# Performance work log

Measured on AMD Instinct MI355X. Metric: run time of the kernel, lower is better.

The kernel has to match this reference:

```python
import jax, jax.numpy as jnp
import numpy as np

NB_ATOMS = 128
NB_CH = 1
ATOM = 12          # atom_size
BATCH = 8
HW = 75            # -> 64x64 patch grid
LAM = 0.1          # soft-threshold level of the L1 proximal
UNROLL = 2         # unroll_steps
FISTA_ITERS = 15   # fixed inner FISTA iterations (replaces res-based stop)


def _prox(u):
    # soft-thresholding (prox of lam*||.||_1)
    return jnp.sign(u) * jnp.maximum(jnp.abs(u) - LAM, 0.0)


def _conv(x, w):
    # valid cross-correlation, NCHW / OIHW (== F.conv2d)
    return jax.lax.conv_general_dilated(x, w, (1, 1), 'VALID',
                                        dimension_numbers=('NCHW', 'OIHW', 'NCHW'))


def _fold(patches, H, W):
    # patches: [B, Ph, Pw, a, a] -> overlap-add to [B, 1, H, W] (== F.fold)
    B, Ph, Pw, a, _ = patches.shape
    out = jnp.zeros((B, H, W), patches.dtype)
    for di in range(a):              # fixed small kernel loop (a*a = 144 slots)
        for dj in range(a):
            out = out.at[:, di:di + Ph, dj:dj + Pw].add(patches[:, :, :, di, dj])
    return out[:, None]


def _fista(c0, X, q, mu):
    # standard FISTA on 0.5*||D^T c - y_patch||^2 + lam*||c||_1 with step mu
    def body(i, st):
        c, z, t = st
        cn = _prox(z - (z @ X - q) * mu)
        tn = (1.0 + jnp.sqrt(1.0 + 4.0 * t * t)) / 2.0
        zn = cn + ((t - 1.0) / tn) * (cn - c)
        return (cn, zn, tn)
    c, _, _ = jax.lax.fori_loop(0, FISTA_ITERS, body, (c0, c0, jnp.float32(1.0)))
    return c


def setup_inputs() -> dict:
    key = jax.random.key(0)
    k1, k2 = jax.random.split(key)
    y = jax.random.normal(k1, (BATCH, NB_CH, HW, HW), dtype=jnp.float32)
    atoms = jax.random.normal(k2, (NB_ATOMS, NB_CH, ATOM, ATOM), dtype=jnp.float32) / 1500.0
    beta = jnp.float32(0.1)
    mu = jnp.float32(1.0)
    return {"y": y, "atoms": atoms, "beta": beta, "mu": mu}


def reference(y, atoms, beta, mu):
    B, C, H, W = y.shape
    N, a = atoms.shape[0], atoms.shape[-1]
    beta = jax.nn.relu(beta)
    mu = jax.nn.relu(mu)
    # normalize atoms: zero-mean, unit L2 rows, then spectral norm / sqrt(mu)
    A = atoms - atoms.mean(axis=(1, 2, 3), keepdims=True)
    Af = A.reshape(N, -1)
    Af = Af / jnp.linalg.norm(Af, axis=1, keepdims=True)
    Af = Af / (jnp.linalg.norm(Af, ord=2) * jnp.sqrt(mu))
    atoms_n = Af.reshape(N, C, a, a)
    X = Af @ Af.T                                   # [N, N] gram
    Ph, Pw = H - a + 1, W - a + 1
    n_patch = B * Ph * Pw
    mean_filter = jnp.ones((1, 1, a, a), y.dtype) / (a * a)
    patch_mean = _conv(y, mean_filter).reshape(n_patch, 1, 1, 1)
    divisors = _fold(jnp.ones((B, Ph, Pw, a, a), y.dtype), H, W)  # overlap counts
    goal = y
    c = jnp.zeros((n_patch, N), y.dtype)
    sg = jax.lax.stop_gradient
    for _ in range(UNROLL):
        q = _conv(goal, atoms_n).transpose(0, 2, 3, 1).reshape(n_patch, N)
        cf = sg(_fista(sg(c), sg(X), sg(q), sg(mu)))   # torch.no_grad inner solve
        cf = _prox(cf - (cf @ X - q) * mu)             # one differentiable step
        pred = jnp.einsum('pn,ncij->pcij', cf, atoms_n) + patch_mean  # [P,1,a,a]
        pred = _fold(pred.reshape(B, Ph, Pw, a, a), H, W)
        goal = (y + beta * pred) / (1.0 + beta * divisors)
        c = cf
    return goal
```

## Files before the change

kernel.cpp:

```cpp
#include <hip/hip_runtime.h>
#include <stdint.h>

#define AA 144
#define LAM 0.1f

#define OFS_SC    0
#define OFS_AF1   64
#define OFS_G     36928
#define OFS_S0    53312
#define OFS_S1    69696
#define OFS_X     86080
#define OFS_PM    139328
#define OFS_GOAL  172096
#define OFS_CF    4411456
#define OFS_PRED  8605760
#define OFS_ATB   OFS_S0
#define OFS_ANTB  OFS_S1


typedef __attribute__((ext_vector_type(8))) short short8_t;
typedef __attribute__((ext_vector_type(4))) float f32x4;
typedef __attribute__((ext_vector_type(2))) float f32x2;
typedef __attribute__((ext_vector_type(4))) uint32_t u32x4;

__device__ __forceinline__ unsigned short f2bf(float f) {
    union { float f; uint32_t u; } x; x.f = f;
    uint32_t u = x.u;
    return (unsigned short)((u + 0x7FFFu + ((u >> 16) & 1u)) >> 16);
}
__device__ __forceinline__ unsigned short f2bh(float f) {
    union { float f; uint32_t u; } x; x.f = f;
    return (unsigned short)((x.u + 0x8000u) >> 16);
}
__device__ __forceinline__ float bf2f(unsigned short u) {
    union { float f; uint32_t i; } x; x.i = ((uint32_t)u) << 16; return x.f;
}
__device__ __forceinline__ uint32_t pack_bf(float a, float b) {
    union { float f; uint32_t u; } xa, xb; xa.f = a; xb.f = b;
    return __builtin_amdgcn_perm(xb.u + 0x8000u, xa.u + 0x8000u, 0x07060302u);
}
__device__ __forceinline__ uint32_t cvt_pk(float a, float b) {
    uint32_t r;
    asm("v_cvt_pk_bf16_f32 %0, %1, %2" : "=v"(r) : "v"(a), "v"(b));
    return r;
}

#define PSTR 136
__global__ __launch_bounds__(1024) void k_setup(const float* atoms, const float* mu_p,
                                                float* ws, const float* y) {
    __shared__ unsigned short ABf[128 * 168];
    __shared__ unsigned short Pb[2][128 * PSTR];
    __shared__ float tr_arr[10];
    __shared__ float v[128];
    __shared__ float red[256];
    int t = threadIdx.x;
    if (blockIdx.x != 0) {
        int e = (blockIdx.x - 1) * 1024 + t;
        if (e < 45000) ws[OFS_GOAL + e] = y[e];
        if (e < 32768) {
            int b = e >> 12, pi = (e >> 6) & 63, pj = e & 63;
            const float* yb = y + b * 5625;
            float s = 0.f;
            for (int di = 0; di < 12; ++di) {
                const float* row = yb + (pi + di) * 75 + pj;
                #pragma unroll
                for (int dj = 0; dj < 12; ++dj) s += row[dj];
            }
            ws[OFS_PM + e] = s * (1.0f / 144.0f);
        }
        return;
    }
    int lane = t & 63, w = t >> 6;
    int col = lane & 15, quad = lane >> 4;
    if (t < 10) tr_arr[t] = (t == 0) ? 128.0f : 0.f;

    {
        int a = t >> 3, sub = t & 7;
        const float* ap = atoms + a * AA + sub * 18;
        float s = 0.f;
        #pragma unroll
        for (int k = 0; k < 18; ++k) s += ap[k];
        s += __shfl_xor(s, 1, 8); s += __shfl_xor(s, 2, 8); s += __shfl_xor(s, 4, 8);
        float mean = s * (1.0f / 144.0f);
        float ss = 0.f;
        #pragma unroll
        for (int k = 0; k < 18; ++k) { float d = ap[k] - mean; ss = fmaf(d, d, ss); }
        ss += __shfl_xor(ss, 1, 8); ss += __shfl_xor(ss, 2, 8); ss += __shfl_xor(ss, 4, 8);
        float rn = 1.0f / sqrtf(ss);
        #pragma unroll
        for (int k = 0; k < 18; ++k) {
            float av = (ap[k] - mean) * rn;
            ws[OFS_AF1 + a * AA + sub * 18 + k] = av;
            ABf[a * 168 + sub * 18 + k] = f2bf(av);
        }
        if (sub == 0) {
            #pragma unroll
            for (int k = AA; k < 160; ++k) ABf[a * 168 + k] = 0;
        }
    }
    __syncthreads();

    {
        uint32_t* D32 = (uint32_t*)Pb[0];
        float* G = ws + OFS_G;
        int mt = w & 7, gh = w >> 3;
        short8_t af[5];
        #pragma unroll
        for (int s = 0; s < 5; ++s)
            af[s] = *(const short8_t*)&ABf[(mt * 16 + col) * 168 + s * 32 + quad * 8];
        #pragma unroll
        for (int gi = 0; gi < 2; ++gi) {
            int g = gh * 2 + gi;
            short8_t b0[5], b1[5];
            #pragma unroll
            for (int s = 0; s < 5; ++s) {
                b0[s] = *(const short8_t*)&ABf[((2 * g) * 16 + col) * 168 + s * 32 + quad * 8];
                b1[s] = *(const short8_t*)&ABf[((2 * g + 1) * 16 + col) * 168 + s * 32 + quad * 8];
            }
            f32x4 a0 = (f32x4){0.f, 0.f, 0.f, 0.f};
            f32x4 a1 = (f32x4){0.f, 0.f, 0.f, 0.f};
            #pragma unroll
            for (int s = 0; s < 5; ++s) {
                a0 = __builtin_amdgcn_mfma_f32_16x16x32_bf16(af[s], b0[s], a0, 0, 0, 0);
                a1 = __builtin_amdgcn_mfma_f32_16x16x32_bf16(af[s], b1[s], a1, 0, 0, 0);
            }
            #pragma unroll
            for (int r = 0; r < 4; ++r) {
                int m = mt * 16 + quad * 4 + r;
                G[m * 128 + g * 32 + col] = a0[r];
                G[m * 128 + g * 32 + 16 + col] = a1[r];
                D32[m * 68 + g * 16 + col] = pack_bf(a0[r], a1[r]);
            }
        }
    }
    __syncthreads();

    int cur = 0;
    #pragma unroll 1
    for (int j = 0; j < 8; ++j) {
        float trn = tr_arr[j];
        float inv2 = 1.0f / (trn * trn);
        const unsigned short* S = Pb[cur];
        uint32_t* D32 = (uint32_t*)Pb[cur ^ 1];
        int mt = w & 7, nh = w >> 3;
        short8_t af[4];
        #pragma unroll
        for (int s = 0; s < 4; ++s)
            af[s] = *(const short8_t*)&S[(mt * 16 + col) * PSTR + s * 32 + quad * 8];
        #pragma unroll
        for (int pr = 0; pr < 2; ++pr) {
            int ntE = 4 * nh + 2 * pr, ntO = ntE + 1;
            short8_t bE[4], bO[4];
            #pragma unroll
            for (int s = 0; s < 4; ++s) {
                bE[s] = *(const short8_t*)&S[(ntE * 16 + col) * PSTR + s * 32 + quad * 8];
                bO[s] = *(const short8_t*)&S[(ntO * 16 + col) * PSTR + s * 32 + quad * 8];
            }
            f32x4 aE = (f32x4){0.f, 0.f, 0.f, 0.f};
            f32x4 aO = (f32x4){0.f, 0.f, 0.f, 0.f};
            #pragma unroll
            for (int s = 0; s < 4; ++s) {
                aE = __builtin_amdgcn_mfma_f32_16x16x32_bf16(af[s], bE[s], aE, 0, 0, 0);
                aO = __builtin_amdgcn_mfma_f32_16x16x32_bf16(af[s], bO[s], aO, 0, 0, 0);
            }
            int nE = ntE * 16 + col, nO = ntO * 16 + col;
            #pragma unroll
            for (int r = 0; r < 4; ++r) {
                float x0 = aE[r] * inv2, x1 = aO[r] * inv2;
                int row = mt * 16 + quad * 4 + r;
                D32[row * 68 + (ntE >> 1) * 16 + col] = pack_bf(x0, x1);
                if (row == nE) atomicAdd(&tr_arr[j + 1], x0);
                if (row == nO) atomicAdd(&tr_arr[j + 1], x1);
            }
        }
        __syncthreads();
        cur ^= 1;
    }

    {
        int a = t >> 3, sub = t & 7;
        const unsigned short* S = Pb[cur];
        float s = 0.f;
        #pragma unroll
        for (int k = 0; k < 16; ++k) s += bf2f(S[a * PSTR + sub * 16 + k]);
        s += __shfl_xor(s, 1, 8); s += __shfl_xor(s, 2, 8); s += __shfl_xor(s, 4, 8);
        if (sub == 0) v[a] = s;
    }
    __syncthreads();
    {
        int a = t >> 3, sub = t & 7;
        const float* G = ws + OFS_G;
        float wv = 0.f;
        #pragma unroll
        for (int k = 0; k < 16; ++k)
            wv = fmaf(G[a * 128 + sub * 16 + k], v[sub * 16 + k], wv);
        wv += __shfl_xor(wv, 1, 8); wv += __shfl_xor(wv, 2, 8); wv += __shfl_xor(wv, 4, 8);
        if (sub == 0) { red[a] = v[a] * wv; red[128 + a] = v[a] * v[a]; }
    }
    __syncthreads();
    for (int off = 64; off > 0; off >>= 1) {
        if (t < off) { red[t] += red[t + off]; red[128 + t] += red[128 + t + off]; }
        __syncthreads();
    }
    if (t == 0) {
        float lam = red[0] / red[128];
        float mu = fmaxf(mu_p[0], 0.0f);
        float scX = 1.0f / (lam * mu);
        float scA = 1.0f / (sqrtf(lam) * sqrtf(mu));
        ws[OFS_SC + 16] = scX * mu;
        ws[OFS_SC + 17] = scA;
        ws[OFS_SC + 18] = -scA * mu;
    }
}

__global__ __launch_bounds__(256) void k_finalize(float* ws) {
    int idx = blockIdx.x * 256 + threadIdx.x;
    float scX = ws[OFS_SC + 16], scA = ws[OFS_SC + 17], scQ = ws[OFS_SC + 18];
    if (idx < 16384) {
        int row = idx >> 7, ks = idx & 127;
        int s = ks >> 5, Q = (ks >> 3) & 3, j = ks & 7;
        int n = 32 * s + 16 * (j >> 2) + 4 * Q + (j & 3);
        ((unsigned short*)(ws + OFS_X))[idx] = f2bf(ws[OFS_G + row * 128 + n] * scX);
    } else if (idx < 36864) {
        int e = idx - 16384;
        int n = e / 160, k = e - n * 160;
        float v = (k < 144) ? ws[OFS_AF1 + n * 144 + k] * scQ : 0.f;
        ((unsigned short*)(ws + OFS_ATB))[e] = f2bf(v);
    } else {
        int e = idx - 36864;
        int jr = e >> 7, ks = e & 127;
        int s = ks >> 5, Q = (ks >> 3) & 3, j = ks & 7;
        int n = 32 * s + 16 * (j >> 2) + 4 * Q + (j & 3);
        ((unsigned short*)(ws + OFS_ANTB))[e] = f2bf(ws[OFS_AF1 + n * 144 + jr] * scA);
    }
}

__global__ __launch_bounds__(256, 4) void k_fista(const unsigned short* XPB,
        const float* goal, const unsigned short* ATB, const unsigned short* ANTBP,
        const float* pm, uint32_t* cfgb, unsigned short* predh,
        int first, int write_cf) {
    __shared__ u32x4 Zx[2][4][64];
    int t = threadIdx.x;
    int lane = t & 63, w = t >> 6;
    int col = lane & 15, Q = lane >> 4;
    int sa = w ^ 1, sb = w ^ 2, sc = w ^ 3;
    int blk = blockIdx.x;
    int b = blk >> 8, pi = (blk >> 2) & 63;
    int pcol = (blk & 3) * 16 + col;
    int p = blk * 16 + col;
    const float* gb = goal + b * 5625 + pi * 75;

    u32x4 bq[5];
    #pragma unroll
    for (int s = 0; s < 5; ++s)
        #pragma unroll
        for (int jj = 0; jj < 4; ++jj) {
            int k0 = 32 * s + 8 * Q + 2 * jj;
            float v0 = 0.f, v1 = 0.f;
            if (k0 < 144) {
                int di = k0 / 12, dj = k0 - di * 12;
                const float* r = gb + di * 75 + pcol + dj;
                v0 = r[0]; v1 = r[1];
            }
            bq[s][jj] = cvt_pk(v0, v1);
        }

    f32x4 qn4[2];
    #pragma unroll
    for (int m = 0; m < 2; ++m) {
        f32x4 a = (f32x4){0.f, 0.f, 0.f, 0.f};
        #pragma unroll
        for (int s = 0; s < 5; ++s) {
            short8_t af = *(const short8_t*)&ATB[((w * 2 + m) * 16 + col) * 160 + 32 * s + 8 * Q];
            a = __builtin_amdgcn_mfma_f32_16x16x32_bf16(af,
                    __builtin_bit_cast(short8_t, bq[s]), a, 0, 0, 0);
        }
        qn4[m] = a;
    }

    short8_t xf_o[2], xf_a[2], xf_b[2], xf_c[2];
    #pragma unroll
    for (int m = 0; m < 2; ++m) {
        const unsigned short* Xr = &XPB[((w * 2 + m) * 16 + col) * 128 + 8 * Q];
        xf_o[m] = *(const short8_t*)&Xr[32 * w];
        xf_a[m] = *(const short8_t*)&Xr[32 * sa];
        xf_b[m] = *(const short8_t*)&Xr[32 * sb];
        xf_c[m] = *(const short8_t*)&Xr[32 * sc];
    }

    f32x2 z2[4], cP[4], cQ[4];
    f32x4 acc4[2];
    u32x4 own, otha, othb, othc;
    if (first) {
        #pragma unroll
        for (int k = 0; k < 4; ++k) { z2[k] = cP[k] = (f32x2){0.f, 0.f}; }
        own = otha = othb = othc = (u32x4){0u, 0u, 0u, 0u};
    } else {
        const u32x4* cp = (const u32x4*)(cfgb + ((size_t)blk * 64 + lane) * 16);
        own = cp[w]; otha = cp[sa]; othb = cp[sb]; othc = cp[sc];
        #pragma unroll
        for (int k = 0; k < 4; ++k) {
            uint32_t pk = own[k];
            cP[k] = (f32x2){__builtin_bit_cast(float, pk << 16),
                            __builtin_bit_cast(float, pk & 0xFFFF0000u)};
            z2[k] = cP[k];
        }
    }

    auto matmul = [&]() {
        #pragma unroll
        for (int m = 0; m < 2; ++m)
            acc4[m] = __builtin_amdgcn_mfma_f32_16x16x32_bf16(xf_o[m],
                          __builtin_bit_cast(short8_t, own), qn4[m], 0, 0, 0);
        #pragma unroll
        for (int m = 0; m < 2; ++m)
            acc4[m] = __builtin_amdgcn_mfma_f32_16x16x32_bf16(xf_a[m],
                          __builtin_bit_cast(short8_t, otha), acc4[m], 0, 0, 0);
        #pragma unroll
        for (int m = 0; m < 2; ++m)
            acc4[m] = __builtin_amdgcn_mfma_f32_16x16x32_bf16(xf_b[m],
                          __builtin_bit_cast(short8_t, othb), acc4[m], 0, 0, 0);
        #pragma unroll
        for (int m = 0; m < 2; ++m)
            acc4[m] = __builtin_amdgcn_mfma_f32_16x16x32_bf16(xf_c[m],
                          __builtin_bit_cast(short8_t, othc), acc4[m], 0, 0, 0);
    };
    auto exchange = [&](int buf) {
        Zx[buf][w][lane] = own;
        __syncthreads();
        otha = Zx[buf][sa][lane];
        othb = Zx[buf][sb][lane];
        othc = Zx[buf][sc][lane];
    };
    auto upd = [&](f32x2 (&cOld)[4], f32x2 (&cNew)[4], float fm) {
        f32x2 fm2 = (f32x2){fm, fm};
        #pragma unroll
        for (int k = 0; k < 4; ++k) {
            f32x2 a2 = (f32x2){acc4[k >> 1][2 * (k & 1)], acc4[k >> 1][2 * (k & 1) + 1]};
            f32x2 u = z2[k] - a2;
            f32x2 cl = (f32x2){__builtin_amdgcn_fmed3f(u[0], -LAM, LAM),
                               __builtin_amdgcn_fmed3f(u[1], -LAM, LAM)};
            f32x2 cn = u - cl;
            cNew[k] = cn;
            f32x2 zn = cn + fm2 * (cn - cOld[k]);
            z2[k] = zn;
            own[k] = cvt_pk(zn[0], zn[1]);
        }
    };
    auto prx = [&](f32x2 (&base)[4], f32x2 (&dst)[4]) {
        #pragma unroll
        for (int k = 0; k < 4; ++k) {
            f32x2 a2 = (f32x2){acc4[k >> 1][2 * (k & 1)], acc4[k >> 1][2 * (k & 1) + 1]};
            f32x2 u = base[k] - a2;
            f32x2 cl = (f32x2){__builtin_amdgcn_fmed3f(u[0], -LAM, LAM),
                               __builtin_amdgcn_fmed3f(u[1], -LAM, LAM)};
            f32x2 cn = u - cl;
            dst[k] = cn;
            own[k] = cvt_pk(cn[0], cn[1]);
        }
    };

    #define ZITER(FM, CO, CN, BUF) do { matmul(); upd(CO, CN, FM); exchange(BUF); } while (0)
    ZITER(0.00000000f, cP, cQ, 0);
    ZITER(0.28175333f, cQ, cP, 1);
    ZITER(0.43404370f, cP, cQ, 0);
    ZITER(0.53106374f, cQ, cP, 1);
    ZITER(0.59877861f, cP, cQ, 0);
    ZITER(0.64892339f, cQ, cP, 1);
    ZITER(0.68764594f, cP, cQ, 0);
    ZITER(0.71850003f, cQ, cP, 1);
    ZITER(0.74369097f, cP, cQ, 0);
    ZITER(0.76466381f, cQ, cP, 1);
    ZITER(0.78240892f, cP, cQ, 0);
    ZITER(0.79762527f, cQ, cP, 1);
    ZITER(0.81081957f, cP, cQ, 0);
    ZITER(0.82237667f, cQ, cP, 1);
    #undef ZITER
    {
        matmul();
        prx(z2, cQ);
        exchange(0);
    }
    {
        matmul();
        prx(cQ, cQ);
        exchange(1);
    }
    if (write_cf) {
        u32x4* cp = (u32x4*)(cfgb + ((size_t)blk * 64 + lane) * 16);
        cp[w] = own;
    }

    {
        float pmv = pm[p];
        f32x4 pm4 = (f32x4){pmv, pmv, pmv, pmv};
        int jm0 = (w == 0) ? 0 : (2 * w + 1);
        int jmN = (w == 0) ? 3 : 2;
        #pragma unroll
        for (int ji = 0; ji < 3; ++ji) {
            if (ji < jmN) {
                int jm = jm0 + ji;
                const unsigned short* Ar = &ANTBP[(jm * 16 + col) * 128 + 8 * Q];
                short8_t an_o = *(const short8_t*)&Ar[32 * w];
                short8_t an_a = *(const short8_t*)&Ar[32 * sa];
                short8_t an_b = *(const short8_t*)&Ar[32 * sb];
                short8_t an_c = *(const short8_t*)&Ar[32 * sc];
                f32x4 a = pm4;
                a = __builtin_amdgcn_mfma_f32_16x16x32_bf16(an_o,
                        __builtin_bit_cast(short8_t, own), a, 0, 0, 0);
                a = __builtin_amdgcn_mfma_f32_16x16x32_bf16(an_a,
                        __builtin_bit_cast(short8_t, otha), a, 0, 0, 0);
                a = __builtin_amdgcn_mfma_f32_16x16x32_bf16(an_b,
                        __builtin_bit_cast(short8_t, othb), a, 0, 0, 0);
                a = __builtin_amdgcn_mfma_f32_16x16x32_bf16(an_c,
                        __builtin_bit_cast(short8_t, othc), a, 0, 0, 0);
                #pragma unroll
                for (int r = 0; r < 4; ++r)
                    predh[(jm * 16 + 4 * Q + r) * 32768 + p] = f2bh(a[r]);
            }
        }
    }
}

__global__ __launch_bounds__(256) void k_fold(const float* y, const float* beta_p,
                                              const unsigned short* predh, float* goal,
                                              float* out, int write_out) {
    __shared__ float P[12 * 832];
    int i = blockIdx.x, b = blockIdx.y;
    int t = threadIdx.x;
    for (int di = 0; di < 12; ++di) {
        int pi = i - di;
        if ((unsigned)pi >= 64u) continue;
        int base = (b << 12) + (pi << 6);
        #pragma unroll
        for (int it = 0; it < 3; ++it) {
            int e = t + it * 256;
            int dj = e >> 6, pj = e & 63;
            P[di * 832 + pj * 13 + dj] = bf2f(predh[(di * 12 + dj) * 32768 + base + pj]);
        }
    }
    __syncthreads();
    if (t >= 75) return;
    int j = t;
    float S = 0.f;
    for (int di = 0; di < 12; ++di) {
        if ((unsigned)(i - di) >= 64u) continue;
        const float* Pd = &P[di * 832];
        #pragma unroll
        for (int dj = 0; dj < 12; ++dj) {
            int pj = j - dj;
            if ((unsigned)pj >= 64u) continue;
            S += Pd[pj * 13 + dj];
        }
    }
    int ci = min(i, 11) - max(i - 63, 0) + 1;
    int cj = min(j, 11) - max(j - 63, 0) + 1;
    float beta = fmaxf(beta_p[0], 0.0f);
    int idx = i * 75 + j;
    float yv = y[b * 5625 + idx];
    float g = (yv + beta * S) / (1.0f + beta * (float)(ci * cj));
    if (write_out) out[b * 5625 + idx] = g;
    else           goal[b * 5625 + idx] = g;
}

extern "C" void kernel_launch(void* const* d_in, const int* in_sizes, int n_in,
                              void* d_out, int out_size, void* d_ws, size_t ws_size,
                              hipStream_t stream) {
    const float* y     = (const float*)d_in[0];
    const float* atoms = (const float*)d_in[1];
    const float* beta  = (const float*)d_in[2];
    const float* mu    = (const float*)d_in[3];
    float* out = (float*)d_out;
    float* ws = (float*)d_ws;

    k_setup<<<46, 1024, 0, stream>>>(atoms, mu, ws, y);
    k_finalize<<<216, 256, 0, stream>>>(ws);

    for (int u = 0; u < 2; ++u) {
        k_fista<<<2048, 256, 0, stream>>>((const unsigned short*)(ws + OFS_X),
                                          ws + OFS_GOAL,
                                          (const unsigned short*)(ws + OFS_ATB),
                                          (const unsigned short*)(ws + OFS_ANTB),
                                          ws + OFS_PM, (uint32_t*)(ws + OFS_CF),
                                          (unsigned short*)(ws + OFS_PRED),
                                          u == 0 ? 1 : 0, u == 0 ? 1 : 0);
        k_fold<<<dim3(75, 8), 256, 0, stream>>>(y, beta,
                                                (const unsigned short*)(ws + OFS_PRED),
                                                ws + OFS_GOAL, out, u == 1 ? 1 : 0);
    }
}
```

Measured before the change: 185.9 us.

## Process two 16-patch tiles per FISTA block to share X fragments and syncs

Each k_fista block now handles 32 patches as two independent 16-column tiles (A and B), halving the grid to 1024 blocks. The X-gram and atom fragments loaded into registers are reused for both tiles, and each iteration's LDS exchange and barrier serve both tiles, so there are half as many barriers per unit of work. The two interleaved MFMA chains can also hide each other's latency. In exchange, register pressure roughly doubles (launch bounds drop from 4 to 3 blocks per SM), occupancy and the number of blocks fall, and LDS use doubles.

```diff
diff --git a/kernel.cpp b/kernel.cpp
--- a/kernel.cpp
+++ b/kernel.cpp
@@ -235,47 +235,53 @@
     }
 }
 
-__global__ __launch_bounds__(256, 4) void k_fista(const unsigned short* XPB,
+__global__ __launch_bounds__(256, 3) void k_fista(const unsigned short* XPB,
         const float* goal, const unsigned short* ATB, const unsigned short* ANTBP,
         const float* pm, uint32_t* cfgb, unsigned short* predh,
         int first, int write_cf) {
-    __shared__ u32x4 Zx[2][4][64];
+    __shared__ u32x4 Zx[2][2][4][64];
     int t = threadIdx.x;
     int lane = t & 63, w = t >> 6;
     int col = lane & 15, Q = lane >> 4;
     int sa = w ^ 1, sb = w ^ 2, sc = w ^ 3;
     int blk = blockIdx.x;
-    int b = blk >> 8, pi = (blk >> 2) & 63;
-    int pcol = (blk & 3) * 16 + col;
-    int p = blk * 16 + col;
+    int b = blk >> 7, pi = (blk >> 1) & 63;
+    int pcA = (blk & 1) * 32 + col;
+    int pA = blk * 32 + col, pB = pA + 16;
     const float* gb = goal + b * 5625 + pi * 75;
 
-    u32x4 bq[5];
+    u32x4 bqA[5], bqB[5];
     #pragma unroll
     for (int s = 0; s < 5; ++s)
         #pragma unroll
         for (int jj = 0; jj < 4; ++jj) {
             int k0 = 32 * s + 8 * Q + 2 * jj;
-            float v0 = 0.f, v1 = 0.f;
+            float a0 = 0.f, a1 = 0.f, b0 = 0.f, b1 = 0.f;
             if (k0 < 144) {
                 int di = k0 / 12, dj = k0 - di * 12;
-                const float* r = gb + di * 75 + pcol + dj;
-                v0 = r[0]; v1 = r[1];
-            }
-            bq[s][jj] = cvt_pk(v0, v1);
-        }
-
-    f32x4 qn4[2];
+                const float* r = gb + di * 75 + pcA + dj;
+                a0 = r[0]; a1 = r[1];
+                b0 = r[16]; b1 = r[17];
+            }
+            bqA[s][jj] = cvt_pk(a0, a1);
+            bqB[s][jj] = cvt_pk(b0, b1);
+        }
+
+    f32x4 qnA[2], qnB[2];
     #pragma unroll
     for (int m = 0; m < 2; ++m) {
-        f32x4 a = (f32x4){0.f, 0.f, 0.f, 0.f};
+        f32x4 aA = (f32x4){0.f, 0.f, 0.f, 0.f};
+        f32x4 aB = (f32x4){0.f, 0.f, 0.f, 0.f};
         #pragma unroll
         for (int s = 0; s < 5; ++s) {
             short8_t af = *(const short8_t*)&ATB[((w * 2 + m) * 16 + col) * 160 + 32 * s + 8 * Q];
-            a = __builtin_amdgcn_mfma_f32_16x16x32_bf16(af,
-                    __builtin_bit_cast(short8_t, bq[s]), a, 0, 0, 0);
-        }
-        qn4[m] = a;
+            aA = __builtin_amdgcn_mfma_f32_16x16x32_bf16(af,
+                     __builtin_bit_cast(short8_t, bqA[s]), aA, 0, 0, 0);
+            aB = __builtin_amdgcn_mfma_f32_16x16x32_bf16(af,
+                     __builtin_bit_cast(short8_t, bqB[s]), aB, 0, 0, 0);
+        }
+        qnA[m] = aA;
+        qnB[m] = aB;
     }
 
     short8_t xf_o[2], xf_a[2], xf_b[2], xf_c[2];
@@ -288,79 +294,101 @@
         xf_c[m] = *(const short8_t*)&Xr[32 * sc];
     }
 
-    f32x2 z2[4], cP[4], cQ[4];
-    f32x4 acc4[2];
-    u32x4 own, otha, othb, othc;
+    f32x2 zA[4], cPA[4], cQA[4], zB[4], cPB[4], cQB[4];
+    f32x4 accA[2], accB[2];
+    u32x4 ownA, othaA, othbA, othcA, ownB, othaB, othbB, othcB;
     if (first) {
         #pragma unroll
-        for (int k = 0; k < 4; ++k) { z2[k] = cP[k] = (f32x2){0.f, 0.f}; }
-        own = otha = othb = othc = (u32x4){0u, 0u, 0u, 0u};
+        for (int k = 0; k < 4; ++k) {
+            zA[k] = cPA[k] = (f32x2){0.f, 0.f};
+            zB[k] = cPB[k] = (f32x2){0.f, 0.f};
+        }
+        ownA = othaA = othbA = othcA = (u32x4){0u, 0u, 0u, 0u};
+        ownB = othaB = othbB = othcB = (u32x4){0u, 0u, 0u, 0u};
     } else {
-        const u32x4* cp = (const u32x4*)(cfgb + ((size_t)blk * 64 + lane) * 16);
-        own = cp[w]; otha = cp[sa]; othb = cp[sb]; othc = cp[sc];
+        const u32x4* cpA = (const u32x4*)(cfgb + ((size_t)(2 * blk) * 64 + lane) * 16);
+        const u32x4* cpB = (const u32x4*)(cfgb + ((size_t)(2 * blk + 1) * 64 + lane) * 16);
+        ownA = cpA[w]; othaA = cpA[sa]; othbA = cpA[sb]; othcA = cpA[sc];
+        ownB = cpB[w]; othaB = cpB[sa]; othbB = cpB[sb]; othcB = cpB[sc];
         #pragma unroll
         for (int k = 0; k < 4; ++k) {
-            uint32_t pk = own[k];
-            cP[k] = (f32x2){__builtin_bit_cast(float, pk << 16),
-                            __builtin_bit_cast(float, pk & 0xFFFF0000u)};
-            z2[k] = cP[k];
-        }
-    }
-
-    auto matmul = [&]() {
+            uint32_t a0 = ownA[k], b0 = ownB[k];
+            cPA[k] = (f32x2){__builtin_bit_cast(float, a0 << 16),
+                             __builtin_bit_cast(float, a0 & 0xFFFF0000u)};
+            cPB[k] = (f32x2){__builtin_bit_cast(float, b0 << 16),
+                             __builtin_bit_cast(float, b0 & 0xFFFF0000u)};
+            zA[k] = cPA[k];
+            zB[k] = cPB[k];
+        }
+    }
+
+    auto matmul = [&](u32x4& o, u32x4& xa_, u32x4& xb_, u32x4& xc_,
+                      f32x4 (&qn)[2], f32x4 (&acc)[2]) {
         #pragma unroll
         for (int m = 0; m < 2; ++m)
-            acc4[m] = __builtin_amdgcn_mfma_f32_16x16x32_bf16(xf_o[m],
-                          __builtin_bit_cast(short8_t, own), qn4[m], 0, 0, 0);
+            acc[m] = __builtin_amdgcn_mfma_f32_16x16x32_bf16(xf_o[m],
+                         __builtin_bit_cast(short8_t, o), qn[m], 0, 0, 0);
         #pragma unroll
         for (int m = 0; m < 2; ++m)
-            acc4[m] = __builtin_amdgcn_mfma_f32_16x16x32_bf16(xf_a[m],
-                          __builtin_bit_cast(short8_t, otha), acc4[m], 0, 0, 0);
+            acc[m] = __builtin_amdgcn_mfma_f32_16x16x32_bf16(xf_a[m],
+                         __builtin_bit_cast(short8_t, xa_), acc[m], 0, 0, 0);
         #pragma unroll
         for (int m = 0; m < 2; ++m)
-            acc4[m] = __builtin_amdgcn_mfma_f32_16x16x32_bf16(xf_b[m],
-                          __builtin_bit_cast(short8_t, othb), acc4[m], 0, 0, 0);
+            acc[m] = __builtin_amdgcn_mfma_f32_16x16x32_bf16(xf_b[m],
+                         __builtin_bit_cast(short8_t, xb_), acc[m], 0, 0, 0);
         #pragma unroll
         for (int m = 0; m < 2; ++m)
-            acc4[m] = __builtin_amdgcn_mfma_f32_16x16x32_bf16(xf_c[m],
-                          __builtin_bit_cast(short8_t, othc), acc4[m], 0, 0, 0);
+            acc[m] = __builtin_amdgcn_mfma_f32_16x16x32_bf16(xf_c[m],
+                         __builtin_bit_cast(short8_t, xc_), acc[m], 0, 0, 0);
     };
     auto exchange = [&](int buf) {
-        Zx[buf][w][lane] = own;
+        Zx[buf][0][w][lane] = ownA;
+        Zx[buf][1][w][lane] = ownB;
         __syncthreads();
-        otha = Zx[buf][sa][lane];
-        othb = Zx[buf][sb][lane];
-        othc = Zx[buf][sc][lane];
+        othaA = Zx[buf][0][sa][lane];
+        othbA = Zx[buf][0][sb][lane];
+        othcA = Zx[buf][0][sc][lane];
+        othaB = Zx[buf][1][sa][lane];
+        othbB = Zx[buf][1][sb][lane];
+        othcB = Zx[buf][1][sc][lane];
     };
-    auto upd = [&](f32x2 (&cOld)[4], f32x2 (&cNew)[4], float fm) {
+    auto upd = [&](f32x2 (&z)[4], f32x2 (&cOld)[4], f32x2 (&cNew)[4],
+                   f32x4 (&acc)[2], u32x4& o, float fm) {
         f32x2 fm2 = (f32x2){fm, fm};
         #pragma unroll
         for (int k = 0; k < 4; ++k) {
-            f32x2 a2 = (f32x2){acc4[k >> 1][2 * (k & 1)], acc4[k >> 1][2 * (k & 1) + 1]};
-            f32x2 u = z2[k] - a2;
+            f32x2 a2 = (f32x2){acc[k >> 1][2 * (k & 1)], acc[k >> 1][2 * (k & 1) + 1]};
+            f32x2 u = z[k] - a2;
             f32x2 cl = (f32x2){__builtin_amdgcn_fmed3f(u[0], -LAM, LAM),
                                __builtin_amdgcn_fmed3f(u[1], -LAM, LAM)};
             f32x2 cn = u - cl;
             cNew[k] = cn;
             f32x2 zn = cn + fm2 * (cn - cOld[k]);
-            z2[k] = zn;
-            own[k] = cvt_pk(zn[0], zn[1]);
+            z[k] = zn;
+            o[k] = cvt_pk(zn[0], zn[1]);
         }
     };
-    auto prx = [&](f32x2 (&base)[4], f32x2 (&dst)[4]) {
+    auto prx = [&](f32x2 (&base)[4], f32x2 (&dst)[4], f32x4 (&acc)[2], u32x4& o) {
         #pragma unroll
         for (int k = 0; k < 4; ++k) {
-            f32x2 a2 = (f32x2){acc4[k >> 1][2 * (k & 1)], acc4[k >> 1][2 * (k & 1) + 1]};
+            f32x2 a2 = (f32x2){acc[k >> 1][2 * (k & 1)], acc[k >> 1][2 * (k & 1) + 1]};
             f32x2 u = base[k] - a2;
             f32x2 cl = (f32x2){__builtin_amdgcn_fmed3f(u[0], -LAM, LAM),
                                __builtin_amdgcn_fmed3f(u[1], -LAM, LAM)};
             f32x2 cn = u - cl;
             dst[k] = cn;
-            own[k] = cvt_pk(cn[0], cn[1]);
+            o[k] = cvt_pk(cn[0], cn[1]);
         }
     };
 
-    #define ZITER(FM, CO, CN, BUF) do { matmul(); upd(CO, CN, FM); exchange(BUF); } while (0)
+    #define ZITER(FM, CO, CN, BUF)                                         \
+        do {                                                               \
+            matmul(ownA, othaA, othbA, othcA, qnA, accA);                  \
+            matmul(ownB, othaB, othbB, othcB, qnB, accB);                  \
+            upd(zA, CO##A, CN##A, accA, ownA, FM);                         \
+            upd(zB, CO##B, CN##B, accB, ownB, FM);                         \
+            exchange(BUF);                                                 \
+        } while (0)
     ZITER(0.00000000f, cP, cQ, 0);
     ZITER(0.28175333f, cQ, cP, 1);
     ZITER(0.43404370f, cP, cQ, 0);
@@ -377,23 +405,30 @@
     ZITER(0.82237667f, cQ, cP, 1);
     #undef ZITER
     {
-        matmul();
-        prx(z2, cQ);
+        matmul(ownA, othaA, othbA, othcA, qnA, accA);
+        matmul(ownB, othaB, othbB, othcB, qnB, accB);
+        prx(zA, cQA, accA, ownA);
+        prx(zB, cQB, accB, ownB);
         exchange(0);
     }
     {
-        matmul();
-        prx(cQ, cQ);
+        matmul(ownA, othaA, othbA, othcA, qnA, accA);
+        matmul(ownB, othaB, othbB, othcB, qnB, accB);
+        prx(cQA, cQA, accA, ownA);
+        prx(cQB, cQB, accB, ownB);
         exchange(1);
     }
     if (write_cf) {
-        u32x4* cp = (u32x4*)(cfgb + ((size_t)blk * 64 + lane) * 16);
-        cp[w] = own;
-    }
-
-    {
-        float pmv = pm[p];
-        f32x4 pm4 = (f32x4){pmv, pmv, pmv, pmv};
+        u32x4* cpA = (u32x4*)(cfgb + ((size_t)(2 * blk) * 64 + lane) * 16);
+        u32x4* cpB = (u32x4*)(cfgb + ((size_t)(2 * blk + 1) * 64 + lane) * 16);
+        cpA[w] = ownA;
+        cpB[w] = ownB;
+    }
+
+    {
+        float pmA = pm[pA], pmB = pm[pB];
+        f32x4 pmA4 = (f32x4){pmA, pmA, pmA, pmA};
+        f32x4 pmB4 = (f32x4){pmB, pmB, pmB, pmB};
         int jm0 = (w == 0) ? 0 : (2 * w + 1);
         int jmN = (w == 0) ? 3 : 2;
         #pragma unroll
@@ -405,18 +440,29 @@
                 short8_t an_a = *(const short8_t*)&Ar[32 * sa];
                 short8_t an_b = *(const short8_t*)&Ar[32 * sb];
                 short8_t an_c = *(const short8_t*)&Ar[32 * sc];
-                f32x4 a = pm4;
+                f32x4 a = pmA4;
                 a = __builtin_amdgcn_mfma_f32_16x16x32_bf16(an_o,
-                        __builtin_bit_cast(short8_t, own), a, 0, 0, 0);
+                        __builtin_bit_cast(short8_t, ownA), a, 0, 0, 0);
                 a = __builtin_amdgcn_mfma_f32_16x16x32_bf16(an_a,
-                        __builtin_bit_cast(short8_t, otha), a, 0, 0, 0);
+                        __builtin_bit_cast(short8_t, othaA), a, 0, 0, 0);
                 a = __builtin_amdgcn_mfma_f32_16x16x32_bf16(an_b,
-                        __builtin_bit_cast(short8_t, othb), a, 0, 0, 0);
+                        __builtin_bit_cast(short8_t, othbA), a, 0, 0, 0);
                 a = __builtin_amdgcn_mfma_f32_16x16x32_bf16(an_c,
-                        __builtin_bit_cast(short8_t, othc), a, 0, 0, 0);
+                        __builtin_bit_cast(short8_t, othcA), a, 0, 0, 0);
+                f32x4 bb = pmB4;
+                bb = __builtin_amdgcn_mfma_f32_16x16x32_bf16(an_o,
+                         __builtin_bit_cast(short8_t, ownB), bb, 0, 0, 0);
+                bb = __builtin_amdgcn_mfma_f32_16x16x32_bf16(an_a,
+                         __builtin_bit_cast(short8_t, othaB), bb, 0, 0, 0);
+                bb = __builtin_amdgcn_mfma_f32_16x16x32_bf16(an_b,
+                         __builtin_bit_cast(short8_t, othbB), bb, 0, 0, 0);
+                bb = __builtin_amdgcn_mfma_f32_16x16x32_bf16(an_c,
+                         __builtin_bit_cast(short8_t, othcB), bb, 0, 0, 0);
                 #pragma unroll
-                for (int r = 0; r < 4; ++r)
-                    predh[(jm * 16 + 4 * Q + r) * 32768 + p] = f2bh(a[r]);
+                for (int r = 0; r < 4; ++r) {
+                    predh[(jm * 16 + 4 * Q + r) * 32768 + pA] = f2bh(a[r]);
+                    predh[(jm * 16 + 4 * Q + r) * 32768 + pB] = f2bh(bb[r]);
+                }
             }
         }
     }
@@ -477,7 +523,7 @@
     k_finalize<<<216, 256, 0, stream>>>(ws);
 
     for (int u = 0; u < 2; ++u) {
-        k_fista<<<2048, 256, 0, stream>>>((const unsigned short*)(ws + OFS_X),
+        k_fista<<<1024, 256, 0, stream>>>((const unsigned short*)(ws + OFS_X),
                                           ws + OFS_GOAL,
                                           (const unsigned short*)(ws + OFS_ATB),
                                           (const unsigned short*)(ws + OFS_ANTB),
```

Measured after the change: 182.2 us (median of 10 runs). 1.02x faster.
